# Kernel optimization log

Measured on AMD Instinct MI355X. Metric: run time of the kernel, lower is better.

The kernel has to match this reference:

```python
import jax, jax.numpy as jnp
import numpy as np

B, N, D = 4, 1024, 512
H, DH = 8, 64
TC, AB = 512, 16
EPS = 1e-5
NEG = 1e6


def setup_inputs() -> dict:
    key = jax.random.key(0)
    ks = jax.random.split(key, 10)
    inp = {
        "x": jax.random.normal(ks[0], (B, N, D), jnp.float32),
        "time": jax.random.normal(ks[1], (B, 1, TC), jnp.float32),
        "attn_bias": jax.random.normal(ks[2], (B, AB, N, N), jnp.float32),
        "seq_mask": jnp.ones((B, N), jnp.float32),
        "gamma": jnp.ones((D,), jnp.float32),
        "Wt": jax.random.normal(ks[3], (2 * D, TC), jnp.float32) * 0.02,
        "bt": jnp.zeros((2 * D,), jnp.float32),
        "Wq": jax.random.normal(ks[4], (H * DH, D), jnp.float32) * 0.02,
        "Wkv": jax.random.normal(ks[5], (2 * H * DH, D), jnp.float32) * 0.02,
        "Wo": jax.random.normal(ks[6], (D, H * DH), jnp.float32) * 0.02,
        "Wb": jax.random.normal(ks[7], (H, AB), jnp.float32) * 0.02,
        "bb": jnp.zeros((H,), jnp.float32),
    }
    return inp


def reference(x, time, attn_bias, seq_mask, gamma, Wt, bt, Wq, Wkv, Wo, Wb, bb):
    # context defaults to raw x BEFORE norm/FiLM/mask (faithful to source order)
    ctx = x
    # LayerNorm (beta buffer is zero)
    mu = jnp.mean(x, axis=-1, keepdims=True)
    var = jnp.mean(jnp.square(x - mu), axis=-1, keepdims=True)
    xn = (x - mu) * jax.lax.rsqrt(var + EPS) * gamma
    # FiLM time conditioning: SiLU -> Linear -> chunk
    t = jax.nn.silu(time) @ Wt.T + bt            # [B,1,2D]
    scale, shift = jnp.split(t, 2, axis=-1)
    xn = xn * (scale + 1.0) + shift
    # seq mask on queries' input
    xn = xn * seq_mask[..., None]
    # projections
    q = xn @ Wq.T                                 # [B,N,H*DH]
    kv = ctx @ Wkv.T                              # [B,N,2*H*DH]
    k, v = jnp.split(kv, 2, axis=-1)
    to_heads = lambda t: t.reshape(B, N, H, DH).transpose(0, 2, 1, 3)
    q, k, v = to_heads(q), to_heads(k), to_heads(v)
    q = q * (DH ** -0.5)
    sim = jnp.einsum('bhid,bhjd->bhij', q, k)     # [B,H,N,N]
    # learned projection of attn_bias channels -> heads
    bias = jnp.einsum('baij,ha->bhij', attn_bias, Wb) + bb[None, :, None, None]
    sim = sim + bias
    m = seq_mask[:, None, :, None] * seq_mask[:, None, None, :]  # [B,1,N,N]
    sim = sim - (1.0 - m) * NEG
    attn = jax.nn.softmax(sim, axis=-1)
    out = jnp.einsum('bhij,bhjd->bhid', attn, v)
    out = out.transpose(0, 2, 1, 3).reshape(B, N, H * DH)
    out = out @ Wo.T
    return out * seq_mask[..., None]
```

## Files before the change

kernel.cpp:

```cpp
#include <hip/hip_runtime.h>
#include <hip/hip_bf16.h>
#include <math.h>

#define B_  4
#define N_  1024
#define D_  512
#define H_  8
#define DH_ 64
#define TC_ 512
#define AB_ 16
#define EPS_ 1e-5f
#define NEG_ 1e6f

typedef _Float16 half8v __attribute__((ext_vector_type(8)));
typedef _Float16 half4v __attribute__((ext_vector_type(4)));
typedef float floatx4 __attribute__((ext_vector_type(4)));

__global__ __launch_bounds__(256)
void film_kernel(const float* __restrict__ time_in,
                 const float* __restrict__ Wt,
                 const float* __restrict__ bt,
                 float* __restrict__ film) {
    __shared__ float st[TC_];
    int b = blockIdx.x >> 8;
    int cblk = blockIdx.x & 255;
    const float* trow = time_in + b * TC_;
    for (int j = threadIdx.x; j < TC_; j += 256) {
        float tv = trow[j];
        st[j] = tv / (1.f + __expf(-tv));
    }
    __syncthreads();
    int wave = threadIdx.x >> 6, lane = threadIdx.x & 63;
    int c = cblk * 4 + wave;
    const float* wrow = Wt + (size_t)c * TC_;
    float acc = 0.f;
    #pragma unroll
    for (int j0 = 0; j0 < TC_; j0 += 64)
        acc += st[j0 + lane] * wrow[j0 + lane];
    #pragma unroll
    for (int off = 32; off; off >>= 1)
        acc += __shfl_down(acc, off);
    if (lane == 0) film[b * 2 * D_ + c] = acc + bt[c];
}

__global__ __launch_bounds__(256)
void cvt_w3_kernel(const float* __restrict__ Wq, const float* __restrict__ Wkv,
                   const float* __restrict__ Wo,
                   _Float16* __restrict__ Wqh, _Float16* __restrict__ Wkvh,
                   _Float16* __restrict__ Woh) {
    int i = blockIdx.x * 256 + threadIdx.x;
    const float* src;
    _Float16* dst;
    float sc = 1.f;
    int off;
    if (i < 65536)       { src = Wq;  dst = Wqh;  off = i;          sc = 0.125f; }
    else if (i < 196608) { src = Wkv; dst = Wkvh; off = i - 65536;  }
    else                 { src = Wo;  dst = Woh;  off = i - 196608; }
    float4 v = ((const float4*)src)[off];
    half4v o;
    o.x = (_Float16)(v.x * sc); o.y = (_Float16)(v.y * sc);
    o.z = (_Float16)(v.z * sc); o.w = (_Float16)(v.w * sc);
    ((half4v*)dst)[off] = o;
}

__global__ __launch_bounds__(256)
void ln_film_kernel(const float* __restrict__ x,
                    const float* __restrict__ gamma,
                    const float* __restrict__ film,
                    const float* __restrict__ seq_mask,
                    _Float16* __restrict__ xnh,
                    _Float16* __restrict__ xh) {
    int row = blockIdx.x;
    int b = row >> 10;
    int t = threadIdx.x;
    const float* xr = x + (size_t)row * D_;
    float v0 = xr[t];
    float v1 = xr[t + 256];
    xh[(size_t)row * D_ + t]       = (_Float16)v0;
    xh[(size_t)row * D_ + t + 256] = (_Float16)v1;
    float s = v0 + v1;
    float sq = v0 * v0 + v1 * v1;
    int lane = t & 63, wave = t >> 6;
    #pragma unroll
    for (int off = 32; off; off >>= 1) {
        s  += __shfl_down(s, off);
        sq += __shfl_down(sq, off);
    }
    __shared__ float rs[4], rq[4];
    if (lane == 0) { rs[wave] = s; rq[wave] = sq; }
    __syncthreads();
    float mu  = (rs[0] + rs[1] + rs[2] + rs[3]) * (1.f / D_);
    float ex2 = (rq[0] + rq[1] + rq[2] + rq[3]) * (1.f / D_);
    float var = ex2 - mu * mu;
    float rstd = rsqrtf(var + EPS_);
    float mrow = seq_mask[row];
    const float* scale = film + (size_t)b * 2 * D_;
    const float* shift = scale + D_;
    {
        int d = t;
        float val = (v0 - mu) * rstd * gamma[d];
        val = val * (scale[d] + 1.f) + shift[d];
        xnh[(size_t)row * D_ + d] = (_Float16)(val * mrow);
    }
    {
        int d = t + 256;
        float val = (v1 - mu) * rstd * gamma[d];
        val = val * (scale[d] + 1.f) + shift[d];
        xnh[(size_t)row * D_ + d] = (_Float16)(val * mrow);
    }
}

#define LDK 40
template <typename OUTT>
__device__ __forceinline__
void gemm_tile(const _Float16* __restrict__ A,
               const _Float16* __restrict__ Bt,
               OUTT* __restrict__ C,
               int M, int Nn, int K, int bx, int by,
               _Float16* As, _Float16* Bs) {
    int t = threadIdx.x;
    int wave = t >> 6, lane = t & 63;
    int quad = lane >> 4, l16 = lane & 15;
    int m0 = by * 128, n0 = bx * 128;
    int wm = (wave >> 1) * 64, wn = (wave & 1) * 64;

    floatx4 acc[4][4];
    #pragma unroll
    for (int i = 0; i < 4; ++i)
        #pragma unroll
        for (int j = 0; j < 4; ++j)
            acc[i][j] = (floatx4){0.f, 0.f, 0.f, 0.f};

    int row0 = t >> 2;
    int seg0 = (t & 3) * 8;

    for (int k0 = 0; k0 < K; k0 += 32) {
        half8v a0 = *(const half8v*)(A  + (size_t)(m0 + row0)      * K + k0 + seg0);
        half8v a1 = *(const half8v*)(A  + (size_t)(m0 + row0 + 64) * K + k0 + seg0);
        half8v b0 = *(const half8v*)(Bt + (size_t)(n0 + row0)      * K + k0 + seg0);
        half8v b1 = *(const half8v*)(Bt + (size_t)(n0 + row0 + 64) * K + k0 + seg0);
        __syncthreads();
        *(half8v*)(As + row0 * LDK + seg0)        = a0;
        *(half8v*)(As + (row0 + 64) * LDK + seg0) = a1;
        *(half8v*)(Bs + row0 * LDK + seg0)        = b0;
        *(half8v*)(Bs + (row0 + 64) * LDK + seg0) = b1;
        __syncthreads();

        half8v af[4], bf[4];
        #pragma unroll
        for (int i = 0; i < 4; ++i)
            af[i] = *(half8v*)(As + (wm + i * 16 + l16) * LDK + quad * 8);
        #pragma unroll
        for (int j = 0; j < 4; ++j)
            bf[j] = *(half8v*)(Bs + (wn + j * 16 + l16) * LDK + quad * 8);
        #pragma unroll
        for (int i = 0; i < 4; ++i)
            #pragma unroll
            for (int j = 0; j < 4; ++j)
                acc[i][j] = __builtin_amdgcn_mfma_f32_16x16x32_f16(
                    af[i], bf[j], acc[i][j], 0, 0, 0);
    }

    #pragma unroll
    for (int i = 0; i < 4; ++i)
        #pragma unroll
        for (int j = 0; j < 4; ++j)
            #pragma unroll
            for (int r = 0; r < 4; ++r) {
                int grow = m0 + wm + i * 16 + quad * 4 + r;
                int gcol = n0 + wn + j * 16 + l16;
                C[(size_t)grow * Nn + gcol] = (OUTT)acc[i][j][r];
            }
}

__global__ __launch_bounds__(256)
void proj3_kernel(const _Float16* __restrict__ xnh,
                  const _Float16* __restrict__ xh,
                  const _Float16* __restrict__ Wqh,
                  const _Float16* __restrict__ Wkvh,
                  _Float16* __restrict__ qh,
                  _Float16* __restrict__ kh,
                  _Float16* __restrict__ vth) {
    __shared__ _Float16 As[128 * LDK];
    __shared__ _Float16 Bs[128 * LDK];
    int z = blockIdx.x;
    if (z < 128) {
        gemm_tile<_Float16>(xnh, Wqh, qh, 4096, 512, 512, z & 3, z >> 2, As, Bs);
    } else if (z < 256) {
        int y = z - 128;
        gemm_tile<_Float16>(xh, Wkvh, kh, 4096, 512, 512, y & 3, y >> 2, As, Bs);
    } else {
        int y = z - 256;
        gemm_tile<_Float16>(Wkvh + 512 * 512, xh, vth, 512, 4096, 512,
                            y & 31, y >> 5, As, Bs);
    }
}

__global__ __launch_bounds__(256)
void gemm_f32_kernel(const _Float16* __restrict__ A,
                     const _Float16* __restrict__ Bt,
                     float* __restrict__ C, int M, int Nn, int K) {
    __shared__ _Float16 As[128 * LDK];
    __shared__ _Float16 Bs[128 * LDK];
    gemm_tile<float>(A, Bt, C, M, Nn, K, blockIdx.x, blockIdx.y, As, Bs);
}

__global__ __launch_bounds__(256)
void bias_proj_kernel(const float* __restrict__ ab,
                      const float* __restrict__ seq_mask,
                      const float* __restrict__ Wb,
                      const float* __restrict__ bb,
                      __hip_bfloat16* __restrict__ pb) {
    __shared__ float wbs[8][16];
    __shared__ float bbs[8];
    int blk = blockIdx.x;
    int b = blk >> 10;
    int i = blk & 1023;
    int t = threadIdx.x;
    if (t < 128) wbs[t >> 4][t & 15] = Wb[t];
    if (t < 8)   bbs[t] = bb[t];
    __syncthreads();

    float accx[8], accy[8], accz[8], accw[8];
    #pragma unroll
    for (int h = 0; h < 8; ++h) { accx[h] = accy[h] = accz[h] = accw[h] = bbs[h]; }

    const float* base = ab + ((size_t)(b * AB_) * N_ + i) * N_ + t * 4;
    #pragma unroll
    for (int a = 0; a < AB_; ++a) {
        float4 v = *(const float4*)(base + (size_t)a * N_ * N_);
        #pragma unroll
        for (int h = 0; h < 8; ++h) {
            float w = wbs[h][a];
            accx[h] += v.x * w;
            accy[h] += v.y * w;
            accz[h] += v.z * w;
            accw[h] += v.w * w;
        }
    }
    float mq = seq_mask[blk];
    float4 mk = *(const float4*)(seq_mask + b * N_ + t * 4);
    float px = (1.f - mq * mk.x) * NEG_;
    float py = (1.f - mq * mk.y) * NEG_;
    float pz = (1.f - mq * mk.z) * NEG_;
    float pw = (1.f - mq * mk.w) * NEG_;

    #pragma unroll
    for (int h = 0; h < 8; ++h) {
        __hip_bfloat16 tmp[4];
        tmp[0] = __float2bfloat16(accx[h] - px);
        tmp[1] = __float2bfloat16(accy[h] - py);
        tmp[2] = __float2bfloat16(accz[h] - pz);
        tmp[3] = __float2bfloat16(accw[h] - pw);
        size_t off = (((size_t)(b * 8 + h) * N_) + i) * N_ + t * 4;
        *(ushort4*)(pb + off) = *(ushort4*)tmp;
    }
}

#define LDF 72
#define LDP 72
#define LDV 72
#define LDB 68
__global__ __launch_bounds__(256)
void flash_mfma_kernel(const _Float16* __restrict__ qh,
                       const _Float16* __restrict__ kh,
                       const _Float16* __restrict__ vth,
                       const unsigned short* __restrict__ pb,
                       const float* __restrict__ seq_mask,
                       _Float16* __restrict__ atth) {
    __shared__ _Float16 Ks[2][64 * LDF];
    __shared__ _Float16 Vt[2][64 * LDV];
    __shared__ _Float16 Ps[64 * LDP];
    __shared__ unsigned short PBs[2][64 * LDB];

    int z  = blockIdx.x;
    int qt = z & 15;
    int h  = (z >> 4) & 7;
    int b  = z >> 7;
    int i0 = qt * 64;
    int t  = threadIdx.x;
    int wave = t >> 6, lane = t & 63;
    int quad = lane >> 4, l16 = lane & 15;
    int strip = wave * 16;

    const _Float16* qbase =
        qh + ((size_t)(b * N_ + i0 + strip + l16)) * 512 + h * 64;
    half8v qf[2];
    qf[0] = *(const half8v*)(qbase + quad * 8);
    qf[1] = *(const half8v*)(qbase + 32 + quad * 8);

    const _Float16* kb0 = kh + (size_t)(b * N_) * 512 + h * 64;
    const _Float16* vb0 = vth + (size_t)(h * 64) * 4096 + b * N_;
    int sr = t >> 3;
    int c8 = (t & 7) * 8;

    int pr_row = t >> 2;
    int pr_col = (t & 3) * 16;
    const unsigned short* pbsrc =
        pb + ((size_t)((b * 8 + h) * N_) + i0 + pr_row) * N_ + pr_col;

    half8v kr[2], vr[2];
    #pragma unroll
    for (int l = 0; l < 2; ++l) {
        int r = l * 32 + sr;
        kr[l] = *(const half8v*)(kb0 + (size_t)r * 512 + c8);
        vr[l] = *(const half8v*)(vb0 + (size_t)r * 4096 + c8);
    }
    uint4 pr0 = *(const uint4*)(pbsrc);
    uint4 pr1 = *(const uint4*)(pbsrc + 8);

    float m_r[4], l_r[4];
    floatx4 acco[4];
    #pragma unroll
    for (int r = 0; r < 4; ++r) { m_r[r] = -1e30f; l_r[r] = 0.f; }
    #pragma unroll
    for (int tl = 0; tl < 4; ++tl)
        acco[tl] = (floatx4){0.f, 0.f, 0.f, 0.f};

    for (int jt = 0; jt < 16; ++jt) {
        int cur = jt & 1;
        _Float16* Ksc = Ks[cur];
        _Float16* Vtc = Vt[cur];
        unsigned short* PBc = PBs[cur];
        #pragma unroll
        for (int l = 0; l < 2; ++l) {
            int r = l * 32 + sr;
            *(half8v*)(Ksc + r * LDF + c8) = kr[l];
            *(half8v*)(Vtc + r * LDV + c8) = vr[l];
        }
        {
            unsigned short* dst = PBc + pr_row * LDB + pr_col;
            *(uint2*)(dst)      = *(uint2*)&pr0;
            *(uint2*)(dst + 4)  = *((uint2*)&pr0 + 1);
            *(uint2*)(dst + 8)  = *(uint2*)&pr1;
            *(uint2*)(dst + 12) = *((uint2*)&pr1 + 1);
        }
        __syncthreads();

        if (jt < 15) {
            int j0n = (jt + 1) * 64;
            #pragma unroll
            for (int l = 0; l < 2; ++l) {
                int r = l * 32 + sr;
                kr[l] = *(const half8v*)(kb0 + (size_t)(j0n + r) * 512 + c8);
                vr[l] = *(const half8v*)(vb0 + (size_t)r * 4096 + j0n + c8);
            }
            pr0 = *(const uint4*)(pbsrc + j0n);
            pr1 = *(const uint4*)(pbsrc + j0n + 8);
        }

        floatx4 accs[4];
        #pragma unroll
        for (int tl = 0; tl < 4; ++tl)
            #pragma unroll
            for (int r = 0; r < 4; ++r)
                accs[tl][r] = __uint_as_float(
                    (unsigned)PBc[(strip + quad * 4 + r) * LDB + tl * 16 + l16] << 16);

        __builtin_amdgcn_s_setprio(1);
        #pragma unroll
        for (int c = 0; c < 2; ++c)
            #pragma unroll
            for (int tl = 0; tl < 4; ++tl) {
                half8v kf = *(half8v*)(Ksc + (tl * 16 + l16) * LDF + c * 32 + quad * 8);
                accs[tl] = __builtin_amdgcn_mfma_f32_16x16x32_f16(
                    qf[c], kf, accs[tl], 0, 0, 0);
            }
        __builtin_amdgcn_s_setprio(0);

        float rm[4];
        #pragma unroll
        for (int r = 0; r < 4; ++r)
            rm[r] = fmaxf(fmaxf(accs[0][r], accs[1][r]),
                          fmaxf(accs[2][r], accs[3][r]));
        #pragma unroll
        for (int off = 1; off < 16; off <<= 1)
            #pragma unroll
            for (int r = 0; r < 4; ++r)
                rm[r] = fmaxf(rm[r], __shfl_xor(rm[r], off));
        float alpha[4], rsum[4], pv[4][4];
        #pragma unroll
        for (int r = 0; r < 4; ++r) {
            float mn = fmaxf(m_r[r], rm[r]);
            alpha[r] = __expf(m_r[r] - mn);
            m_r[r] = mn;
            float s = 0.f;
            #pragma unroll
            for (int tl = 0; tl < 4; ++tl) {
                float e = __expf(accs[tl][r] - mn);
                pv[tl][r] = e;
                s += e;
            }
            rsum[r] = s;
        }
        #pragma unroll
        for (int off = 1; off < 16; off <<= 1)
            #pragma unroll
            for (int r = 0; r < 4; ++r)
                rsum[r] += __shfl_xor(rsum[r], off);
        #pragma unroll
        for (int r = 0; r < 4; ++r) {
            l_r[r] = l_r[r] * alpha[r] + rsum[r];
            #pragma unroll
            for (int tl = 0; tl < 4; ++tl) {
                acco[tl][r] *= alpha[r];
                Ps[(strip + quad * 4 + r) * LDP + tl * 16 + l16] =
                    (_Float16)pv[tl][r];
            }
        }

        __builtin_amdgcn_s_setprio(1);
        #pragma unroll
        for (int c = 0; c < 2; ++c) {
            half8v pf = *(half8v*)(Ps + (strip + l16) * LDP + c * 32 + quad * 8);
            #pragma unroll
            for (int tl = 0; tl < 4; ++tl) {
                half8v vf = *(half8v*)(Vtc + (tl * 16 + l16) * LDV + c * 32 + quad * 8);
                acco[tl] = __builtin_amdgcn_mfma_f32_16x16x32_f16(
                    pf, vf, acco[tl], 0, 0, 0);
            }
        }
        __builtin_amdgcn_s_setprio(0);
    }

    #pragma unroll
    for (int r = 0; r < 4; ++r) {
        int row = i0 + strip + quad * 4 + r;
        float msk = seq_mask[b * N_ + row];
        float inv = msk / l_r[r];
        _Float16* ob = atth + ((size_t)(b * N_ + row)) * 512 + h * 64;
        #pragma unroll
        for (int tl = 0; tl < 4; ++tl)
            ob[tl * 16 + l16] = (_Float16)(acco[tl][r] * inv);
    }
}

extern "C" void kernel_launch(void* const* d_in, const int* in_sizes, int n_in,
                              void* d_out, int out_size, void* d_ws, size_t ws_size,
                              hipStream_t stream) {
    const float* x         = (const float*)d_in[0];
    const float* time_in   = (const float*)d_in[1];
    const float* attn_bias = (const float*)d_in[2];
    const float* seq_mask  = (const float*)d_in[3];
    const float* gamma     = (const float*)d_in[4];
    const float* Wt        = (const float*)d_in[5];
    const float* bt        = (const float*)d_in[6];
    const float* Wq        = (const float*)d_in[7];
    const float* Wkv       = (const float*)d_in[8];
    const float* Wo        = (const float*)d_in[9];
    const float* Wb        = (const float*)d_in[10];
    const float* bb        = (const float*)d_in[11];
    float* out = (float*)d_out;

    char* ws = (char*)d_ws;
    const size_t KB = 1024, MB = 1024 * 1024;
    float*     film = (float*)ws;
    _Float16*  xnh  = (_Float16*)(ws + 16 * KB);
    _Float16*  xh   = (_Float16*)(ws + 16 * KB + 4 * MB);
    _Float16*  Wqh  = (_Float16*)(ws + 16 * KB + 8 * MB);
    _Float16*  Wkvh = (_Float16*)(ws + 16 * KB + 8 * MB + 512 * KB);
    _Float16*  Woh  = (_Float16*)(ws + 16 * KB + 9 * MB + 512 * KB);
    _Float16*  qh   = (_Float16*)(ws + 16 * KB + 10 * MB);
    _Float16*  kh   = (_Float16*)(ws + 16 * KB + 14 * MB);
    _Float16*  vth  = (_Float16*)(ws + 16 * KB + 18 * MB);
    _Float16*  atth = (_Float16*)(ws + 16 * KB + 22 * MB);
    __hip_bfloat16* pb = (__hip_bfloat16*)(ws + 16 * KB + 26 * MB);

    film_kernel<<<1024, 256, 0, stream>>>(time_in, Wt, bt, film);
    ln_film_kernel<<<4096, 256, 0, stream>>>(x, gamma, film, seq_mask, xnh, xh);
    cvt_w3_kernel<<<1024, 256, 0, stream>>>(Wq, Wkv, Wo, Wqh, Wkvh, Woh);

    proj3_kernel<<<384, 256, 0, stream>>>(xnh, xh, Wqh, Wkvh, qh, kh, vth);

    bias_proj_kernel<<<4096, 256, 0, stream>>>(attn_bias, seq_mask, Wb, bb, pb);
    flash_mfma_kernel<<<512, 256, 0, stream>>>(qh, kh, vth,
                                               (const unsigned short*)pb,
                                               seq_mask, atth);

    dim3 go(512 / 128, 4096 / 128);
    gemm_f32_kernel<<<go, 256, 0, stream>>>(atth, Woh, out, 4096, 512, 512);
}
```

Baseline: 468.3 us.

## Merge FiLM and weight-convert kernels, retile output GEMM, move flash barrier

Combines the FiLM projection and the fp16 weight conversion into one launch to save a kernel launch. Replaces the output projection GEMM with a dedicated 128x64-tile kernel, which doubles the block count from 128 to 256 so more CUs have work. In the flash attention loop, the barrier after the shared-memory stores now comes after the next tile's global prefetch loads are issued, so the loads can be in flight while the barrier waits. The new GEMM has no register prefetch of the next k-slice and may expose more load latency.

```diff
diff --git a/kernel.cpp b/kernel.cpp
--- a/kernel.cpp
+++ b/kernel.cpp
@@ -17,50 +17,50 @@
 typedef float floatx4 __attribute__((ext_vector_type(4)));
 
 __global__ __launch_bounds__(256)
-void film_kernel(const float* __restrict__ time_in,
-                 const float* __restrict__ Wt,
-                 const float* __restrict__ bt,
-                 float* __restrict__ film) {
+void film_cvtw_kernel(const float* __restrict__ time_in,
+                      const float* __restrict__ Wt,
+                      const float* __restrict__ bt,
+                      float* __restrict__ film,
+                      const float* __restrict__ Wq, const float* __restrict__ Wkv,
+                      const float* __restrict__ Wo,
+                      _Float16* __restrict__ Wqh, _Float16* __restrict__ Wkvh,
+                      _Float16* __restrict__ Woh) {
     __shared__ float st[TC_];
-    int b = blockIdx.x >> 8;
-    int cblk = blockIdx.x & 255;
-    const float* trow = time_in + b * TC_;
-    for (int j = threadIdx.x; j < TC_; j += 256) {
-        float tv = trow[j];
-        st[j] = tv / (1.f + __expf(-tv));
-    }
-    __syncthreads();
-    int wave = threadIdx.x >> 6, lane = threadIdx.x & 63;
-    int c = cblk * 4 + wave;
-    const float* wrow = Wt + (size_t)c * TC_;
-    float acc = 0.f;
-    #pragma unroll
-    for (int j0 = 0; j0 < TC_; j0 += 64)
-        acc += st[j0 + lane] * wrow[j0 + lane];
-    #pragma unroll
-    for (int off = 32; off; off >>= 1)
-        acc += __shfl_down(acc, off);
-    if (lane == 0) film[b * 2 * D_ + c] = acc + bt[c];
-}
-
-__global__ __launch_bounds__(256)
-void cvt_w3_kernel(const float* __restrict__ Wq, const float* __restrict__ Wkv,
-                   const float* __restrict__ Wo,
-                   _Float16* __restrict__ Wqh, _Float16* __restrict__ Wkvh,
-                   _Float16* __restrict__ Woh) {
-    int i = blockIdx.x * 256 + threadIdx.x;
-    const float* src;
-    _Float16* dst;
-    float sc = 1.f;
-    int off;
-    if (i < 65536)       { src = Wq;  dst = Wqh;  off = i;          sc = 0.125f; }
-    else if (i < 196608) { src = Wkv; dst = Wkvh; off = i - 65536;  }
-    else                 { src = Wo;  dst = Woh;  off = i - 196608; }
-    float4 v = ((const float4*)src)[off];
-    half4v o;
-    o.x = (_Float16)(v.x * sc); o.y = (_Float16)(v.y * sc);
-    o.z = (_Float16)(v.z * sc); o.w = (_Float16)(v.w * sc);
-    ((half4v*)dst)[off] = o;
+    if (blockIdx.x < 1024) {
+        int b = blockIdx.x >> 8;
+        int cblk = blockIdx.x & 255;
+        const float* trow = time_in + b * TC_;
+        for (int j = threadIdx.x; j < TC_; j += 256) {
+            float tv = trow[j];
+            st[j] = tv / (1.f + __expf(-tv));
+        }
+        __syncthreads();
+        int wave = threadIdx.x >> 6, lane = threadIdx.x & 63;
+        int c = cblk * 4 + wave;
+        const float* wrow = Wt + (size_t)c * TC_;
+        float acc = 0.f;
+        #pragma unroll
+        for (int j0 = 0; j0 < TC_; j0 += 64)
+            acc += st[j0 + lane] * wrow[j0 + lane];
+        #pragma unroll
+        for (int off = 32; off; off >>= 1)
+            acc += __shfl_down(acc, off);
+        if (lane == 0) film[b * 2 * D_ + c] = acc + bt[c];
+    } else {
+        int i = (blockIdx.x - 1024) * 256 + threadIdx.x;
+        const float* src;
+        _Float16* dst;
+        float sc = 1.f;
+        int off;
+        if (i < 65536)       { src = Wq;  dst = Wqh;  off = i;          sc = 0.125f; }
+        else if (i < 196608) { src = Wkv; dst = Wkvh; off = i - 65536;  }
+        else                 { src = Wo;  dst = Woh;  off = i - 196608; }
+        float4 v = ((const float4*)src)[off];
+        half4v o;
+        o.x = (_Float16)(v.x * sc); o.y = (_Float16)(v.y * sc);
+        o.z = (_Float16)(v.z * sc); o.w = (_Float16)(v.w * sc);
+        ((half4v*)dst)[off] = o;
+    }
 }
 
 __global__ __launch_bounds__(256)
@@ -197,12 +197,63 @@
 }
 
 __global__ __launch_bounds__(256)
-void gemm_f32_kernel(const _Float16* __restrict__ A,
+void gemm_out_kernel(const _Float16* __restrict__ A,
                      const _Float16* __restrict__ Bt,
-                     float* __restrict__ C, int M, int Nn, int K) {
+                     float* __restrict__ C) {
     __shared__ _Float16 As[128 * LDK];
-    __shared__ _Float16 Bs[128 * LDK];
-    gemm_tile<float>(A, Bt, C, M, Nn, K, blockIdx.x, blockIdx.y, As, Bs);
+    __shared__ _Float16 Bs[64 * LDK];
+    const int K = 512, Nn = 512;
+    int t = threadIdx.x;
+    int wave = t >> 6, lane = t & 63;
+    int quad = lane >> 4, l16 = lane & 15;
+    int m0 = blockIdx.y * 128, n0 = blockIdx.x * 64;
+    int wm = (wave >> 1) * 64, wn = (wave & 1) * 32;
+
+    floatx4 acc[4][2];
+    #pragma unroll
+    for (int i = 0; i < 4; ++i)
+        #pragma unroll
+        for (int j = 0; j < 2; ++j)
+            acc[i][j] = (floatx4){0.f, 0.f, 0.f, 0.f};
+
+    int row0 = t >> 2;
+    int seg0 = (t & 3) * 8;
+
+    for (int k0 = 0; k0 < K; k0 += 32) {
+        half8v a0 = *(const half8v*)(A  + (size_t)(m0 + row0)      * K + k0 + seg0);
+        half8v a1 = *(const half8v*)(A  + (size_t)(m0 + row0 + 64) * K + k0 + seg0);
+        half8v b0 = *(const half8v*)(Bt + (size_t)(n0 + row0)      * K + k0 + seg0);
+        __syncthreads();
+        *(half8v*)(As + row0 * LDK + seg0)        = a0;
+        *(half8v*)(As + (row0 + 64) * LDK + seg0) = a1;
+        *(half8v*)(Bs + row0 * LDK + seg0)        = b0;
+        __syncthreads();
+
+        half8v af[4], bf[2];
+        #pragma unroll
+        for (int i = 0; i < 4; ++i)
+            af[i] = *(half8v*)(As + (wm + i * 16 + l16) * LDK + quad * 8);
+        #pragma unroll
+        for (int j = 0; j < 2; ++j)
+            bf[j] = *(half8v*)(Bs + (wn + j * 16 + l16) * LDK + quad * 8);
+        #pragma unroll
+        for (int i = 0; i < 4; ++i)
+            #pragma unroll
+            for (int j = 0; j < 2; ++j)
+                acc[i][j] = __builtin_amdgcn_mfma_f32_16x16x32_f16(
+                    af[i], bf[j], acc[i][j], 0, 0, 0);
+    }
+
+    #pragma unroll
+    for (int i = 0; i < 4; ++i)
+        #pragma unroll
+        for (int j = 0; j < 2; ++j)
+            #pragma unroll
+            for (int r = 0; r < 4; ++r) {
+                int grow = m0 + wm + i * 16 + quad * 4 + r;
+                int gcol = n0 + wn + j * 16 + l16;
+                C[(size_t)grow * Nn + gcol] = acc[i][j][r];
+            }
 }
 
 __global__ __launch_bounds__(256)
@@ -335,8 +386,6 @@
             *(uint2*)(dst + 8)  = *(uint2*)&pr1;
             *(uint2*)(dst + 12) = *((uint2*)&pr1 + 1);
         }
-        __syncthreads();
-
         if (jt < 15) {
             int j0n = (jt + 1) * 64;
             #pragma unroll
@@ -348,6 +397,7 @@
             pr0 = *(const uint4*)(pbsrc + j0n);
             pr1 = *(const uint4*)(pbsrc + j0n + 8);
         }
+        __syncthreads();
 
         floatx4 accs[4];
         #pragma unroll
@@ -466,17 +516,17 @@
     _Float16*  atth = (_Float16*)(ws + 16 * KB + 22 * MB);
     __hip_bfloat16* pb = (__hip_bfloat16*)(ws + 16 * KB + 26 * MB);
 
-    film_kernel<<<1024, 256, 0, stream>>>(time_in, Wt, bt, film);
+    film_cvtw_kernel<<<2048, 256, 0, stream>>>(time_in, Wt, bt, film,
+                                               Wq, Wkv, Wo, Wqh, Wkvh, Woh);
     ln_film_kernel<<<4096, 256, 0, stream>>>(x, gamma, film, seq_mask, xnh, xh);
-    cvt_w3_kernel<<<1024, 256, 0, stream>>>(Wq, Wkv, Wo, Wqh, Wkvh, Woh);
 
     proj3_kernel<<<384, 256, 0, stream>>>(xnh, xh, Wqh, Wkvh, qh, kh, vth);
-
     bias_proj_kernel<<<4096, 256, 0, stream>>>(attn_bias, seq_mask, Wb, bb, pb);
+
     flash_mfma_kernel<<<512, 256, 0, stream>>>(qh, kh, vth,
                                                (const unsigned short*)pb,
                                                seq_mask, atth);
 
-    dim3 go(512 / 128, 4096 / 128);
-    gemm_f32_kernel<<<go, 256, 0, stream>>>(atth, Woh, out, 4096, 512, 512);
-}
+    dim3 go(512 / 64, 4096 / 128);
+    gemm_out_kernel<<<go, 256, 0, stream>>>(atth, Woh, out);
+}
```

New measurement: 462.8 us. About the same (-1.2%).
